# Performance work log

Hardware: AMD Instinct MI355X
Metric: run time of the kernel (lower is better)

## Reference

```python
import jax, jax.numpy as jnp
import numpy as np

N = 20000   # nodes
E = 240000  # edges (avg degree 12)
D = 128     # hidden_dim
H = 4       # heads
C = D // H  # head dim = 32
L = 3       # layers


def _ln(x, g, b):
    m = x.mean(-1, keepdims=True)
    v = ((x - m) ** 2).mean(-1, keepdims=True)
    return (x - m) / jnp.sqrt(v + 1e-5) * g + b


def setup_inputs() -> dict:
    key = jax.random.key(0)
    ks = iter(jax.random.split(key, 64))
    def w(shape, s=0.02):
        return jax.random.normal(next(ks), shape, jnp.float32) * s
    z = lambda shape: jnp.zeros(shape, jnp.float32)
    o = lambda shape: jnp.ones(shape, jnp.float32)
    inp = {
        'xyz': jax.random.normal(next(ks), (N, 3), jnp.float32) * 10.0,
        'attr': jax.random.uniform(next(ks), (N, 1), jnp.float32),
        'edge_index': jax.random.randint(next(ks), (2, E), 0, N, jnp.int32),
        # input encoder
        'enc_W': w((4, D)), 'enc_b': z((D,)), 'enc_g': o((D,)), 'enc_bb': z((D,)),
        # relative position MLP
        'pos_W1': w((3, D)), 'pos_b1': z((D,)), 'pos_g': o((D,)), 'pos_bb': z((D,)),
        'pos_W2': w((D, D)), 'pos_b2': z((D,)),
        # TransformerConv per-layer params (stacked over L)
        'Wq': w((L, D, D)), 'bq': z((L, D)),
        'Wk': w((L, D, D)), 'bk': z((L, D)),
        'Wv': w((L, D, D)), 'bv': z((L, D)),
        'We': w((L, D, D)),                 # lin_edge (no bias in PyG)
        'Wskip': w((L, D, D)), 'bskip': z((L, D)),
        'Wbeta': w((L, 3 * D, 1)),          # lin_beta (no bias)
        'ln1_g': o((L, D)), 'ln1_b': z((L, D)),
        'ln2_g': o((L, D)), 'ln2_b': z((L, D)),
        'fW1': w((L, D, 2 * D)), 'fb1': z((L, 2 * D)),
        'fW2': w((L, 2 * D, D)), 'fb2': z((L, D)),
        # heads
        'cls_W1': w((D, D // 2)), 'cls_b1': z((D // 2,)),
        'cls_W2': w((D // 2, 4)), 'cls_b2': z((4,)),
        'box_W1': w((D, D // 2)), 'box_b1': z((D // 2,)),
        'box_W2': w((D // 2, 7)), 'box_b2': z((7,)),
    }
    return inp


def reference(xyz, attr, edge_index, enc_W, enc_b, enc_g, enc_bb,
              pos_W1, pos_b1, pos_g, pos_bb, pos_W2, pos_b2,
              Wq, bq, Wk, bk, Wv, bv, We, Wskip, bskip, Wbeta,
              ln1_g, ln1_b, ln2_g, ln2_b, fW1, fb1, fW2, fb2,
              cls_W1, cls_b1, cls_W2, cls_b2, box_W1, box_b1, box_W2, box_b2):
    n = xyz.shape[0]
    src, dst = edge_index[0], edge_index[1]  # x_j = x[src], x_i = x[dst]; aggregate at dst
    inv_sqrt_c = 1.0 / float(np.sqrt(C))

    # input encoder: Linear -> LayerNorm -> ReLU
    x = jnp.concatenate([xyz, attr], axis=-1)
    x = jax.nn.relu(_ln(x @ enc_W + enc_b, enc_g, enc_bb))

    # relative position encoding per edge: i, j = edge_index; rel = xyz[j] - xyz[i]
    rel = xyz[dst] - xyz[src]
    e = jax.nn.relu(_ln(rel @ pos_W1 + pos_b1, pos_g, pos_bb)) @ pos_W2 + pos_b2  # [E, D]

    for l in range(L):
        # TransformerConv (beta=True, concat=True, edge_dim=D), eval mode (no dropout)
        q = (x @ Wq[l] + bq[l]).reshape(n, H, C)
        k = (x @ Wk[l] + bk[l]).reshape(n, H, C)
        v = (x @ Wv[l] + bv[l]).reshape(n, H, C)
        ee = (e @ We[l]).reshape(-1, H, C)          # [E, H, C]
        kj = k[src] + ee                             # edge-conditioned keys
        alpha = (q[dst] * kj).sum(-1) * inv_sqrt_c   # [E, H]
        amax = jax.ops.segment_max(alpha, dst, num_segments=n)
        ex = jnp.exp(alpha - amax[dst])
        den = jax.ops.segment_sum(ex, dst, num_segments=n)
        a = ex / den[dst]                            # scatter softmax over in-edges of dst
        msg = (v[src] + ee) * a[:, :, None]
        out = jax.ops.segment_sum(msg, dst, num_segments=n).reshape(n, D)
        # beta-gated skip
        r = x @ Wskip[l] + bskip[l]
        beta = jax.nn.sigmoid(jnp.concatenate([out, r, out - r], axis=-1) @ Wbeta[l])  # [N,1]
        out = beta * r + (1.0 - beta) * out
        # residual + LN + FFN + residual + LN
        x = _ln(out + x, ln1_g[l], ln1_b[l])
        h = jax.nn.gelu(x @ fW1[l] + fb1[l], approximate=False) @ fW2[l] + fb2[l]
        x = _ln(h + x, ln2_g[l], ln2_b[l])

    cls_logits = jax.nn.relu(x @ cls_W1 + cls_b1) @ cls_W2 + cls_b2  # [N, 4]
    box_pred = jax.nn.relu(x @ box_W1 + box_b1) @ box_W2 + box_b2    # [N, 7]
    return (cls_logits, box_pred)
```

## Files before the change

### kernel.cpp

```cpp
#include <hip/hip_runtime.h>
#include <hip/hip_bf16.h>
#include <math.h>

#define DD 128

typedef __attribute__((ext_vector_type(8))) short short8;
typedef __attribute__((ext_vector_type(4))) float f32x4;


__device__ __forceinline__ unsigned short f2b(float f) {
    unsigned u = __float_as_uint(f);
    return (unsigned short)((u + 0x7FFFu + ((u >> 16) & 1u)) >> 16);
}
__device__ __forceinline__ float b2f(unsigned short b) {
    return __uint_as_float(((unsigned)b) << 16);
}
__device__ __forceinline__ unsigned packbf(float a, float b) {
    return (unsigned)f2b(a) | ((unsigned)f2b(b) << 16);
}

__device__ __forceinline__ void redsum2_half(float& a, float& b) {
    #pragma unroll
    for (int off = 32; off > 0; off >>= 1) {
        a += __shfl_down(a, off);
        b += __shfl_down(b, off);
    }
    __shared__ float sa[4], sb4[4];
    int w = threadIdx.x >> 6;
    if ((threadIdx.x & 63) == 0) { sa[w] = a; sb4[w] = b; }
    __syncthreads();
    int h = threadIdx.x >> 7;
    a = sa[2 * h] + sa[2 * h + 1];
    b = sb4[2 * h] + sb4[2 * h + 1];
    __syncthreads();
}

__global__ __launch_bounds__(256) void setup1_kernel(
        const float* __restrict__ xyz, const float* __restrict__ attr,
        const float* __restrict__ encW, const float* __restrict__ encb,
        const float* __restrict__ encg, const float* __restrict__ encbb,
        float* __restrict__ x, unsigned short* __restrict__ xbuf,
        const float* __restrict__ posW1, const float* __restrict__ posb1,
        const float* __restrict__ posg, float* __restrict__ pw,
        const int* __restrict__ ei, int* __restrict__ deg,
        int N, int E, int encBlocks) {
    const int b = blockIdx.x, t = threadIdx.x;
    if (b < encBlocks) {
        const int h = t >> 7, d = t & 127;
        const int node = b * 2 + h;
        const bool ok = node < N;
        __shared__ float sin4[2][4];
        if (ok && d < 3) sin4[h][d] = xyz[node * 3 + d];
        if (ok && d == 3) sin4[h][3] = attr[node];
        __syncthreads();
        float y = encb[d];
        if (ok) {
            #pragma unroll
            for (int kk = 0; kk < 4; ++kk) y += sin4[h][kk] * encW[kk * DD + d];
        }
        float s = y, s2 = y * y;
        redsum2_half(s, s2);
        if (ok) {
            float mean = s * (1.0f / DD);
            float var = s2 * (1.0f / DD) - mean * mean;
            float xn = fmaxf((y - mean) * rsqrtf(var + 1e-5f) * encg[d] + encbb[d], 0.f);
            x[(size_t)node * DD + d] = xn;
            xbuf[(size_t)node * DD + d] = f2b(xn);
        }
    } else if (b == encBlocks) {
        const int d = t & 127;
        float w0 = posW1[d], w1 = posW1[DD + d], w2 = posW1[2 * DD + d], bb = posb1[d];
        float s0 = w0, s1 = w1;
        redsum2_half(s0, s1);
        float s2 = w2, s3 = bb;
        redsum2_half(s2, s3);
        float c0 = w0 - s0 * (1.f / DD), c1 = w1 - s1 * (1.f / DD);
        float c2 = w2 - s2 * (1.f / DD), bc = bb - s3 * (1.f / DD);
        float gd = posg[d];
        pw[d] = c0 * gd; pw[DD + d] = c1 * gd; pw[2 * DD + d] = c2 * gd; pw[3 * DD + d] = bc * gd;
        float p0 = c0 * c0, p1 = c0 * c1; redsum2_half(p0, p1);
        float p2 = c0 * c2, p3 = c1 * c1; redsum2_half(p2, p3);
        float p4 = c1 * c2, p5 = c2 * c2; redsum2_half(p4, p5);
        float p6 = c0 * bc, p7 = c1 * bc; redsum2_half(p6, p7);
        float p8 = c2 * bc, p9 = bc * bc; redsum2_half(p8, p9);
        if ((t & 127) == 0) {
            pw[512] = p0 * (1.f / DD); pw[513] = p1 * (1.f / DD); pw[514] = p2 * (1.f / DD);
            pw[515] = p3 * (1.f / DD); pw[516] = p4 * (1.f / DD); pw[517] = p5 * (1.f / DD);
            pw[518] = p6 * (1.f / DD); pw[519] = p7 * (1.f / DD); pw[520] = p8 * (1.f / DD);
            pw[521] = p9 * (1.f / DD);
        }
    } else {
        int e = (b - encBlocks - 1) * 256 + t;
        if (e < E) atomicAdd(&deg[ei[E + e]], 1);
    }
}

__global__ void scan_kernel(const int* __restrict__ deg, int* __restrict__ ptr, int n) {
    __shared__ int partial[1024];
    int t = threadIdx.x;
    int CH = (n + 1023) >> 10;
    int beg = t * CH;
    int end = beg + CH; if (end > n) end = n;
    int s = 0;
    for (int i = beg; i < end; ++i) s += deg[i];
    partial[t] = s;
    __syncthreads();
    for (int off = 1; off < 1024; off <<= 1) {
        int add = (t >= off) ? partial[t - off] : 0;
        __syncthreads();
        partial[t] += add;
        __syncthreads();
    }
    int base = (t == 0) ? 0 : partial[t - 1];
    for (int i = beg; i < end; ++i) {
        ptr[i] = base;
        base += deg[i];
    }
    if (end == n && beg < n) ptr[n] = base;
}

__global__ __launch_bounds__(256) void setup2_kernel(
        const int* __restrict__ ei, const float* __restrict__ xyz,
        const float* __restrict__ pw, const int* __restrict__ ptr,
        int* __restrict__ cur, int* __restrict__ cs_src, float4* __restrict__ rel4, int E,
        const float* __restrict__ W2, const float* __restrict__ b2,
        const float* __restrict__ We, unsigned* __restrict__ W2Wep, float* __restrict__ b2We,
        const float* __restrict__ Wq, const float* __restrict__ Wk,
        const float* __restrict__ Wv, const float* __restrict__ Ws,
        const float* __restrict__ fW1, const float* __restrict__ fW2,
        unsigned* __restrict__ Wpall,
        const float* __restrict__ cW1, const float* __restrict__ bW1,
        unsigned* __restrict__ Whp,
        const float* __restrict__ cb1, const float* __restrict__ bb1,
        float* __restrict__ b1cat, int SC) {
    const int b = blockIdx.x, t = threadIdx.x;
    if (b < SC) {
        int e = b * 256 + t;
        if (e >= E) return;
        int srcn = ei[e], dstn = ei[E + e];
        int p = atomicAdd(&cur[dstn], 1);
        int slot = ptr[dstn] + p;
        cs_src[slot] = srcn;
        float r0 = xyz[dstn * 3]     - xyz[srcn * 3];
        float r1 = xyz[dstn * 3 + 1] - xyz[srcn * 3 + 1];
        float r2 = xyz[dstn * 3 + 2] - xyz[srcn * 3 + 2];
        float var = pw[512] * r0 * r0 + pw[515] * r1 * r1 + pw[517] * r2 * r2
                  + 2.f * (pw[513] * r0 * r1 + pw[514] * r0 * r2 + pw[516] * r1 * r2)
                  + 2.f * (pw[518] * r0 + pw[519] * r1 + pw[520] * r2) + pw[521];
        rel4[slot] = make_float4(r0, r1, r2, rsqrtf(var + 1e-5f));
        return;
    }
    if (b < SC + 99) {
        int z = b - SC;
        int y = z / 33, bp = z % 33;
        int sub = t >> 7, d = t & 127;
        int bid = bp * 2 + sub;
        const float* We_l = We + (size_t)y * DD * DD;
        __shared__ float s0[2][DD], s1[2][DD];
        if (bid < 64)       { s0[sub][d] = W2[(2 * bid) * DD + d]; s1[sub][d] = W2[(2 * bid + 1) * DD + d]; }
        else if (bid == 64) { s0[sub][d] = b2[d]; s1[sub][d] = 0.f; }
        __syncthreads();
        if (bid <= 64) {
            float a0 = 0.f, a1 = 0.f;
            #pragma unroll 8
            for (int kk = 0; kk < DD; ++kk) {
                float w = We_l[kk * DD + d];
                a0 += s0[sub][kk] * w;
                a1 += s1[sub][kk] * w;
            }
            if (bid < 64) W2Wep[y * 8192 + (((d << 6) + bid) ^ ((d & 7) << 2))] = packbf(a0, a1);
            else          b2We[y * DD + d] = a0;
        }
        return;
    }
    if (b < SC + 99 + 768) {
        int z = b - SC - 99;
        int blob = z >> 5, bp = z & 31;
        int kp = bp * 2 + (t >> 7), d = t & 127;
        float w0, w1;
        if (blob < 12) {
            int l = blob >> 2, wt = blob & 3;
            const float* W = (wt == 0 ? Wq : wt == 1 ? Wk : wt == 2 ? Wv : Ws) + (size_t)l * DD * DD;
            w0 = W[(size_t)(2 * kp) * DD + d];
            w1 = W[(size_t)(2 * kp + 1) * DD + d];
        } else if (blob < 18) {
            int i = blob - 12, l = i >> 1, hf = i & 1;
            const float* W = fW1 + (size_t)l * DD * 256;
            w0 = W[(size_t)(2 * kp) * 256 + hf * 128 + d];
            w1 = W[(size_t)(2 * kp + 1) * 256 + hf * 128 + d];
        } else {
            int i = blob - 18, l = i >> 1, c = i & 1;
            const float* W = fW2 + (size_t)l * 256 * DD;
            w0 = W[(size_t)(c * 128 + 2 * kp) * DD + d];
            w1 = W[(size_t)(c * 128 + 2 * kp + 1) * DD + d];
        }
        Wpall[blob * 8192 + (((d << 6) + kp) ^ ((d & 7) << 2))] = packbf(w0, w1);
        return;
    }
    if (b < SC + 99 + 768 + 32) {
        int bp = b - (SC + 99 + 768);
        int kp = bp * 2 + (t >> 7), d = t & 127;
        int k0 = 2 * kp, k1 = 2 * kp + 1;
        float w0 = (d < 64) ? cW1[k0 * 64 + d] : bW1[k0 * 64 + (d - 64)];
        float w1 = (d < 64) ? cW1[k1 * 64 + d] : bW1[k1 * 64 + (d - 64)];
        Whp[((d << 6) + kp) ^ ((d & 7) << 2)] = packbf(w0, w1);
        return;
    }
    if (t < 128) b1cat[t] = (t < 64) ? cb1[t] : bb1[t - 64];
}

struct B4 { const float* b[4]; };

__global__ __launch_bounds__(256) void proj_kernel(
        const unsigned short* __restrict__ xb, const unsigned* __restrict__ Wp4, B4 bias,
        unsigned short* __restrict__ qkv, float* __restrict__ rbuf, int rowsN, int rtN,
        const float4* __restrict__ rel4, const float* __restrict__ pw,
        const float* __restrict__ bbp, const unsigned* __restrict__ Wpee,
        const float* __restrict__ biasee, unsigned short* __restrict__ eeout,
        int rowsE, int rtE) {
    __shared__ unsigned Bt[8192];
    __shared__ float sc[640];
    const int t = threadIdx.x;
    const int lane = t & 63, wid = t >> 6;
    const int kqo = (lane >> 4) * 8;

    if ((int)blockIdx.x < rtE) {
        const int rowBase = (int)blockIdx.x << 6;
        #pragma unroll
        for (int i = 0; i < 8; ++i)
            *(uint4*)&Bt[(i * 256 + t) * 4] = *(const uint4*)&Wpee[(i * 256 + t) * 4];
        for (int i = t; i < 640; i += 256)
            sc[i] = (i < 512) ? pw[i] : bbp[i - 512];
        int arow = rowBase + wid * 16 + (lane & 15);
        if (arow > rowsE - 1) arow = rowsE - 1;
        float4 rv = rel4[arow];
        __syncthreads();
        short8 a[4];
        #pragma unroll
        for (int kc = 0; kc < 4; ++kc) {
            union { short8 s; unsigned short u[8]; } cv;
            #pragma unroll
            for (int j = 0; j < 8; ++j) {
                int d = kc * 32 + kqo + j;
                float y = fmaf(rv.x, sc[d], fmaf(rv.y, sc[128 + d], fmaf(rv.z, sc[256 + d], sc[384 + d])));
                cv.u[j] = f2b(fmaxf(fmaf(y, rv.w, sc[512 + d]), 0.f));
            }
            a[kc] = cv.s;
        }
        f32x4 acc[8];
        #pragma unroll
        for (int i = 0; i < 8; ++i) acc[i] = (f32x4){0.f, 0.f, 0.f, 0.f};
        #pragma unroll
        for (int ng = 0; ng < 8; ++ng) {
            int col = ng * 16 + (lane & 15);
            #pragma unroll
            for (int kc = 0; kc < 4; ++kc) {
                int kidx = kc * 16 + (lane >> 4) * 4;
                const short8 b = *(const short8*)((const char*)Bt +
                        ((((col << 6) + kidx) ^ ((col & 7) << 2)) << 2));
                acc[ng] = __builtin_amdgcn_mfma_f32_16x16x32_bf16(a[kc], b, acc[ng], 0, 0, 0);
            }
        }
        __syncthreads();
        unsigned short* sb16 = (unsigned short*)Bt;
        #pragma unroll
        for (int ng = 0; ng < 8; ++ng) {
            int col = ng * 16 + (lane & 15);
            float bv = biasee[col];
            int cp = col >> 1, cb = col & 1;
            #pragma unroll
            for (int r = 0; r < 4; ++r) {
                int row = wid * 16 + (lane >> 4) * 4 + r;
                sb16[((row << 6) + (cp ^ ((row & 7) << 2))) * 2 + cb] = f2b(acc[ng][r] + bv);
            }
        }
        __syncthreads();
        unsigned* outw = (unsigned*)eeout;
        #pragma unroll
        for (int i = 0; i < 4; ++i) {
            int j = i * 1024 + t * 4;
            int row = j >> 6, cp = j & 63;
            uint4 v = *(const uint4*)&Bt[(row << 6) + (cp ^ ((row & 7) << 2))];
            int grow = rowBase + row;
            if (grow < rowsE) *(uint4*)&outw[(size_t)grow * 64 + cp] = v;
        }
        return;
    }

    int bidx = (int)blockIdx.x - rtE;
    const int y = bidx / rtN;
    const int rowBase = (bidx % rtN) << 6;
    const unsigned* Wp = Wp4 + y * 8192;
    #pragma unroll
    for (int i = 0; i < 8; ++i)
        *(uint4*)&Bt[(i * 256 + t) * 4] = *(const uint4*)&Wp[(i * 256 + t) * 4];
    int arow = rowBase + wid * 16 + (lane & 15);
    if (arow > rowsN - 1) arow = rowsN - 1;
    short8 a[4];
    #pragma unroll
    for (int kc = 0; kc < 4; ++kc)
        a[kc] = *(const short8*)(xb + (size_t)arow * DD + kc * 32 + kqo);
    __syncthreads();
    f32x4 acc[8];
    #pragma unroll
    for (int i = 0; i < 8; ++i) acc[i] = (f32x4){0.f, 0.f, 0.f, 0.f};
    #pragma unroll
    for (int ng = 0; ng < 8; ++ng) {
        int col = ng * 16 + (lane & 15);
        #pragma unroll
        for (int kc = 0; kc < 4; ++kc) {
            int kidx = kc * 16 + (lane >> 4) * 4;
            const short8 b = *(const short8*)((const char*)Bt +
                    ((((col << 6) + kidx) ^ ((col & 7) << 2)) << 2));
            acc[ng] = __builtin_amdgcn_mfma_f32_16x16x32_bf16(a[kc], b, acc[ng], 0, 0, 0);
        }
    }
    const float* bs = bias.b[y];
    if (y == 3) {
        #pragma unroll
        for (int ng = 0; ng < 8; ++ng) {
            int col = ng * 16 + (lane & 15);
            float bv = bs[col];
            #pragma unroll
            for (int r = 0; r < 4; ++r) {
                int grow = rowBase + wid * 16 + (lane >> 4) * 4 + r;
                if (grow < rowsN) rbuf[(size_t)grow * DD + col] = acc[ng][r] + bv;
            }
        }
        return;
    }
    __syncthreads();
    unsigned short* sb16 = (unsigned short*)Bt;
    #pragma unroll
    for (int ng = 0; ng < 8; ++ng) {
        int col = ng * 16 + (lane & 15);
        float bv = bs[col];
        int cp = col >> 1, cb = col & 1;
        #pragma unroll
        for (int r = 0; r < 4; ++r) {
            int row = wid * 16 + (lane >> 4) * 4 + r;
            sb16[((row << 6) + (cp ^ ((row & 7) << 2))) * 2 + cb] = f2b(acc[ng][r] + bv);
        }
    }
    __syncthreads();
    unsigned* outw = (unsigned*)qkv;
    #pragma unroll
    for (int i = 0; i < 4; ++i) {
        int j = i * 1024 + t * 4;
        int row = j >> 6, cp = j & 63;
        uint4 v = *(const uint4*)&Bt[(row << 6) + (cp ^ ((row & 7) << 2))];
        int grow = rowBase + row;
        if (grow < rowsN) *(uint4*)&outw[(size_t)grow * 192 + (y << 6) + cp] = v;
    }
}

__global__ __launch_bounds__(256) void aggc_kernel(
        const unsigned* __restrict__ qkv, const unsigned* __restrict__ ee,
        const int* __restrict__ ptr, const int* __restrict__ cs_src,
        const float* __restrict__ r, const float* __restrict__ Wb,
        const float* __restrict__ g1, const float* __restrict__ b1,
        float* __restrict__ x, unsigned* __restrict__ xbw, int N) {
    const int wave = threadIdx.x >> 6;
    const int lane = threadIdx.x & 63;
    const int node = blockIdx.x;
    __shared__ float sS[4];
    __shared__ float sA0[4][64];
    __shared__ float sA1[4][64];

    unsigned qp = qkv[(size_t)node * 192 + lane];
    float q0 = b2f((unsigned short)qp), q1 = b2f((unsigned short)(qp >> 16));
    int beg = ptr[node], end = ptr[node + 1];
    float s = 0.f, a0 = 0.f, a1 = 0.f;
    int idx = beg + wave;
    unsigned epN = 0, kpN = 0, vpN = 0;
    if (idx < end) {
        int j = cs_src[idx];
        epN = __builtin_nontemporal_load(&ee[(size_t)idx * 64 + lane]);
        kpN = qkv[(size_t)j * 192 + 64 + lane];
        vpN = qkv[(size_t)j * 192 + 128 + lane];
    }
    for (; idx < end; idx += 4) {
        unsigned ep = epN, kp = kpN, vp = vpN;
        int nidx = idx + 4;
        if (nidx < end) {
            int jn = cs_src[nidx];
            epN = __builtin_nontemporal_load(&ee[(size_t)nidx * 64 + lane]);
            kpN = qkv[(size_t)jn * 192 + 64 + lane];
            vpN = qkv[(size_t)jn * 192 + 128 + lane];
        }
        float e0 = b2f((unsigned short)ep), e1 = b2f((unsigned short)(ep >> 16));
        float kj0 = b2f((unsigned short)kp) + e0;
        float kj1 = b2f((unsigned short)(kp >> 16)) + e1;
        float p = q0 * kj0 + q1 * kj1;
        p += __shfl_xor(p, 1); p += __shfl_xor(p, 2);
        p += __shfl_xor(p, 4); p += __shfl_xor(p, 8);
        float w = __expf(p * 0.17677669529663687f);
        s += w;
        a0 += (b2f((unsigned short)vp) + e0) * w;
        a1 += (b2f((unsigned short)(vp >> 16)) + e1) * w;
    }
    sS[wave] = s;
    sA0[wave][lane] = a0;
    sA1[wave][lane] = a1;
    __syncthreads();
    if (wave != 0) return;
    s  = sS[0] + sS[1] + sS[2] + sS[3];
    a0 = sA0[0][lane] + sA0[1][lane] + sA0[2][lane] + sA0[3][lane];
    a1 = sA1[0][lane] + sA1[1][lane] + sA1[2][lane] + sA1[3][lane];

    float inv_s = (s > 0.f) ? 1.f / s : 0.f;
    float od0 = a0 * inv_s, od1 = a1 * inv_s;
    float2 rd = *(const float2*)&r[(size_t)node * DD + lane * 2];
    float2 wb0 = *(const float2*)&Wb[lane * 2];
    float2 wb1 = *(const float2*)&Wb[DD + lane * 2];
    float2 wb2 = *(const float2*)&Wb[2 * DD + lane * 2];
    float part = od0 * wb0.x + rd.x * wb1.x + (od0 - rd.x) * wb2.x
               + od1 * wb0.y + rd.y * wb1.y + (od1 - rd.y) * wb2.y;
    #pragma unroll
    for (int m = 1; m < 64; m <<= 1) part += __shfl_xor(part, m);
    float beta = 1.f / (1.f + __expf(-part));
    float2 xo = *(const float2*)&x[(size_t)node * DD + lane * 2];
    float t0 = beta * rd.x + (1.f - beta) * od0 + xo.x;
    float t1 = beta * rd.y + (1.f - beta) * od1 + xo.y;
    float ss = t0 + t1, ss2 = t0 * t0 + t1 * t1;
    #pragma unroll
    for (int m = 1; m < 64; m <<= 1) { ss += __shfl_xor(ss, m); ss2 += __shfl_xor(ss2, m); }
    float mean = ss * (1.f / DD);
    float var = ss2 * (1.f / DD) - mean * mean;
    float inv = rsqrtf(var + 1e-5f);
    float2 gg = *(const float2*)&g1[lane * 2];
    float2 bbv = *(const float2*)&b1[lane * 2];
    float2 res;
    res.x = (t0 - mean) * inv * gg.x + bbv.x;
    res.y = (t1 - mean) * inv * gg.y + bbv.y;
    *(float2*)&x[(size_t)node * DD + lane * 2] = res;
    xbw[(size_t)node * 64 + lane] = packbf(res.x, res.y);
}

__global__ __launch_bounds__(256) void ffn_fused(
        const unsigned short* __restrict__ xbin, const unsigned* __restrict__ Wp1,
        const float* __restrict__ b1f, const unsigned* __restrict__ Wp2,
        const float* __restrict__ b2f, const float* __restrict__ g,
        const float* __restrict__ bbn, float* __restrict__ x,
        unsigned short* __restrict__ xb, int rows) {
    __shared__ unsigned Bt[8192];
    __shared__ unsigned h1t[8192];
    const int t = threadIdx.x;
    const int rowBase = blockIdx.x << 6;
    const int lane = t & 63, wid = t >> 6;
    const int kqo = (lane >> 4) * 8;
    int arow = rowBase + wid * 16 + (lane & 15);
    if (arow > rows - 1) arow = rows - 1;

    short8 a[4];
    #pragma unroll
    for (int kc = 0; kc < 4; ++kc)
        a[kc] = *(const short8*)(xbin + (size_t)arow * DD + kc * 32 + kqo);

    unsigned short* h16 = (unsigned short*)h1t;
    for (int half = 0; half < 2; ++half) {
        if (half) __syncthreads();
        const unsigned* Wp = Wp1 + half * 8192;
        #pragma unroll
        for (int i = 0; i < 8; ++i)
            *(uint4*)&Bt[(i * 256 + t) * 4] = *(const uint4*)&Wp[(i * 256 + t) * 4];
        __syncthreads();
        f32x4 acc[8];
        #pragma unroll
        for (int i = 0; i < 8; ++i) acc[i] = (f32x4){0.f, 0.f, 0.f, 0.f};
        #pragma unroll
        for (int ng = 0; ng < 8; ++ng) {
            int col = ng * 16 + (lane & 15);
            #pragma unroll
            for (int kc = 0; kc < 4; ++kc) {
                int kidx = kc * 16 + (lane >> 4) * 4;
                const short8 b = *(const short8*)((const char*)Bt +
                        ((((col << 6) + kidx) ^ ((col & 7) << 2)) << 2));
                acc[ng] = __builtin_amdgcn_mfma_f32_16x16x32_bf16(a[kc], b, acc[ng], 0, 0, 0);
            }
        }
        #pragma unroll
        for (int ng = 0; ng < 8; ++ng) {
            int col = half * 128 + ng * 16 + (lane & 15);
            float bv = b1f[col];
            int cp = col >> 1, cb = col & 1;
            #pragma unroll
            for (int r = 0; r < 4; ++r) {
                int row = wid * 16 + (lane >> 4) * 4 + r;
                float val = acc[ng][r] + bv;
                val = 0.5f * val * (1.f + erff(val * 0.70710678118654752f));
                h16[((row << 7) + (cp ^ ((row & 7) << 2))) * 2 + cb] = f2b(val);
            }
        }
    }
    f32x4 accF[8];
    #pragma unroll
    for (int i = 0; i < 8; ++i) accF[i] = (f32x4){0.f, 0.f, 0.f, 0.f};
    const int lrow = wid * 16 + (lane & 15);
    for (int c = 0; c < 2; ++c) {
        __syncthreads();
        const unsigned* Wp = Wp2 + c * 8192;
        #pragma unroll
        for (int i = 0; i < 8; ++i)
            *(uint4*)&Bt[(i * 256 + t) * 4] = *(const uint4*)&Wp[(i * 256 + t) * 4];
        __syncthreads();
        short8 ah[4];
        #pragma unroll
        for (int kc = 0; kc < 4; ++kc) {
            int cp4 = c * 64 + kc * 16 + (lane >> 4) * 4;
            ah[kc] = *(const short8*)&h1t[(lrow << 7) + (cp4 ^ ((lrow & 7) << 2))];
        }
        #pragma unroll
        for (int ng = 0; ng < 8; ++ng) {
            int col = ng * 16 + (lane & 15);
            #pragma unroll
            for (int kc = 0; kc < 4; ++kc) {
                int kidx = kc * 16 + (lane >> 4) * 4;
                const short8 b = *(const short8*)((const char*)Bt +
                        ((((col << 6) + kidx) ^ ((col & 7) << 2)) << 2));
                accF[ng] = __builtin_amdgcn_mfma_f32_16x16x32_bf16(ah[kc], b, accF[ng], 0, 0, 0);
            }
        }
    }
    float tt[8][4];
    float rs[4] = {0.f, 0.f, 0.f, 0.f}, rs2[4] = {0.f, 0.f, 0.f, 0.f};
    #pragma unroll
    for (int ng = 0; ng < 8; ++ng) {
        int col = ng * 16 + (lane & 15);
        float bv = b2f[col];
        #pragma unroll
        for (int r = 0; r < 4; ++r) {
            int grow = rowBase + wid * 16 + (lane >> 4) * 4 + r;
            float xo = (grow < rows) ? x[(size_t)grow * DD + col] : 0.f;
            float v = accF[ng][r] + bv + xo;
            tt[ng][r] = v;
            rs[r] += v;
            rs2[r] += v * v;
        }
    }
    #pragma unroll
    for (int r = 0; r < 4; ++r) {
        #pragma unroll
        for (int m = 1; m < 16; m <<= 1) {
            rs[r] += __shfl_xor(rs[r], m);
            rs2[r] += __shfl_xor(rs2[r], m);
        }
    }
    __syncthreads();
    unsigned short* sb16 = (unsigned short*)Bt;
    #pragma unroll
    for (int ng = 0; ng < 8; ++ng) {
        int col = ng * 16 + (lane & 15);
        float gg = g[col], bbb = bbn[col];
        int cp = col >> 1, cb = col & 1;
        #pragma unroll
        for (int r = 0; r < 4; ++r) {
            int grow = rowBase + wid * 16 + (lane >> 4) * 4 + r;
            float mean = rs[r] * (1.f / DD);
            float var = rs2[r] * (1.f / DD) - mean * mean;
            float val = (tt[ng][r] - mean) * rsqrtf(var + 1e-5f) * gg + bbb;
            if (grow < rows) x[(size_t)grow * DD + col] = val;
            int row = wid * 16 + (lane >> 4) * 4 + r;
            sb16[((row << 6) + (cp ^ ((row & 7) << 2))) * 2 + cb] = f2b(val);
        }
    }
    __syncthreads();
    unsigned* outw = (unsigned*)xb;
    #pragma unroll
    for (int i = 0; i < 4; ++i) {
        int j = i * 1024 + t * 4;
        int row = j >> 6, cp = j & 63;
        uint4 v = *(const uint4*)&Bt[(row << 6) + (cp ^ ((row & 7) << 2))];
        int grow = rowBase + row;
        if (grow < rows) *(uint4*)&outw[(size_t)grow * 64 + cp] = v;
    }
}

__global__ __launch_bounds__(256) void heads_fused(
        const unsigned short* __restrict__ xb, const unsigned* __restrict__ Whp,
        const float* __restrict__ b1cat, const float* __restrict__ cW2,
        const float* __restrict__ cb2, const float* __restrict__ bW2,
        const float* __restrict__ bb2, float* __restrict__ outc,
        float* __restrict__ outb, int rows) {
    __shared__ unsigned Bt[8192];
    __shared__ unsigned ht[4096];
    const int t = threadIdx.x;
    const int rowBase = blockIdx.x << 6;
    const int lane = t & 63, wid = t >> 6;
    const int kqo = (lane >> 4) * 8;
    #pragma unroll
    for (int i = 0; i < 8; ++i)
        *(uint4*)&Bt[(i * 256 + t) * 4] = *(const uint4*)&Whp[(i * 256 + t) * 4];
    int arow = rowBase + wid * 16 + (lane & 15);
    if (arow > rows - 1) arow = rows - 1;
    short8 a[4];
    #pragma unroll
    for (int kc = 0; kc < 4; ++kc)
        a[kc] = *(const short8*)(xb + (size_t)arow * DD + kc * 32 + kqo);
    __syncthreads();
    f32x4 acc[8];
    #pragma unroll
    for (int i = 0; i < 8; ++i) acc[i] = (f32x4){0.f, 0.f, 0.f, 0.f};
    #pragma unroll
    for (int ng = 0; ng < 8; ++ng) {
        int col = ng * 16 + (lane & 15);
        #pragma unroll
        for (int kc = 0; kc < 4; ++kc) {
            int kidx = kc * 16 + (lane >> 4) * 4;
            const short8 b = *(const short8*)((const char*)Bt +
                    ((((col << 6) + kidx) ^ ((col & 7) << 2)) << 2));
            acc[ng] = __builtin_amdgcn_mfma_f32_16x16x32_bf16(a[kc], b, acc[ng], 0, 0, 0);
        }
    }
    unsigned short* h16 = (unsigned short*)ht;
    #pragma unroll
    for (int ng = 0; ng < 8; ++ng) {
        int col = ng * 16 + (lane & 15);
        float bv = b1cat[col];
        int cp = col >> 1, cb = col & 1;
        #pragma unroll
        for (int r = 0; r < 4; ++r) {
            int row = wid * 16 + (lane >> 4) * 4 + r;
            h16[((row << 6) + (cp ^ ((row & 7) << 2))) * 2 + cb] = f2b(fmaxf(acc[ng][r] + bv, 0.f));
        }
    }
    __syncthreads();
    for (int i = t; i < 704; i += 256) {
        int n = i / 11, j = i % 11;
        int grow = rowBase + n;
        if (grow >= rows) continue;
        int sw = (n & 7) << 2;
        if (j < 4) {
            float accv = cb2[j];
            #pragma unroll 8
            for (int kp = 0; kp < 32; ++kp) {
                unsigned w = ht[(n << 6) + (kp ^ sw)];
                accv += b2f((unsigned short)w) * cW2[(2 * kp) * 4 + j];
                accv += b2f((unsigned short)(w >> 16)) * cW2[(2 * kp + 1) * 4 + j];
            }
            outc[(size_t)grow * 4 + j] = accv;
        } else {
            int jj = j - 4;
            float accv = bb2[jj];
            #pragma unroll 8
            for (int kp = 0; kp < 32; ++kp) {
                unsigned w = ht[(n << 6) + ((32 + kp) ^ sw)];
                accv += b2f((unsigned short)w) * bW2[(2 * kp) * 7 + jj];
                accv += b2f((unsigned short)(w >> 16)) * bW2[(2 * kp + 1) * 7 + jj];
            }
            outb[(size_t)grow * 7 + jj] = accv;
        }
    }
}

extern "C" void kernel_launch(void* const* d_in, const int* in_sizes, int n_in,
                              void* d_out, int out_size, void* d_ws, size_t ws_size,
                              hipStream_t stream) {
    const float* xyz   = (const float*)d_in[0];
    const float* attr  = (const float*)d_in[1];
    const int*   ei    = (const int*)d_in[2];
    const float* encW  = (const float*)d_in[3];
    const float* encb  = (const float*)d_in[4];
    const float* encg  = (const float*)d_in[5];
    const float* encbb = (const float*)d_in[6];
    const float* posW1 = (const float*)d_in[7];
    const float* posb1 = (const float*)d_in[8];
    const float* posg  = (const float*)d_in[9];
    const float* posbb = (const float*)d_in[10];
    const float* posW2 = (const float*)d_in[11];
    const float* posb2 = (const float*)d_in[12];
    const float* Wq    = (const float*)d_in[13];
    const float* bq    = (const float*)d_in[14];
    const float* Wk    = (const float*)d_in[15];
    const float* bk    = (const float*)d_in[16];
    const float* Wv    = (const float*)d_in[17];
    const float* bv    = (const float*)d_in[18];
    const float* We    = (const float*)d_in[19];
    const float* Wskip = (const float*)d_in[20];
    const float* bskip = (const float*)d_in[21];
    const float* Wbeta = (const float*)d_in[22];
    const float* ln1g  = (const float*)d_in[23];
    const float* ln1b  = (const float*)d_in[24];
    const float* ln2g  = (const float*)d_in[25];
    const float* ln2b  = (const float*)d_in[26];
    const float* fW1   = (const float*)d_in[27];
    const float* fb1   = (const float*)d_in[28];
    const float* fW2   = (const float*)d_in[29];
    const float* fb2   = (const float*)d_in[30];
    const float* cW1   = (const float*)d_in[31];
    const float* cb1   = (const float*)d_in[32];
    const float* cW2   = (const float*)d_in[33];
    const float* cb2   = (const float*)d_in[34];
    const float* bW1   = (const float*)d_in[35];
    const float* bb1   = (const float*)d_in[36];
    const float* bW2   = (const float*)d_in[37];
    const float* bb2   = (const float*)d_in[38];

    const int N = in_sizes[0] / 3;
    const int E = in_sizes[2] / 2;

    size_t off = 0;
    auto alloc = [&](size_t nelem) {
        char* p = (char*)d_ws + off;
        off += nelem * sizeof(float);
        return (float*)p;
    };
    float* x     = alloc((size_t)N * DD);
    unsigned short* qkv = (unsigned short*)alloc((size_t)N * 192);
    float* r     = alloc((size_t)N * DD);
    unsigned short* xb = (unsigned short*)alloc((size_t)N * 64);
    float4* rel4 = (float4*)alloc((size_t)E * 4);
    unsigned short* eeb = (unsigned short*)alloc((size_t)E * 64);
    unsigned* W2Wep = (unsigned*)alloc(3 * 8192);
    float* b2We  = alloc(3 * DD);
    unsigned* Wpall = (unsigned*)alloc(24 * 8192);
    unsigned* Whp   = (unsigned*)alloc(8192);
    float* pw    = alloc(544);
    float* b1cat = alloc(DD);
    int* deg     = (int*)alloc(N);
    int* cur     = (int*)alloc(N);
    int* ptr     = (int*)alloc(N + 1);
    int* cs_src  = (int*)alloc(E);

    const int rtN = (N + 63) / 64;
    const int rtE = (E + 63) / 64;
    const int encBlocks = (N + 1) / 2;
    const int SC = (E + 255) / 256;

    hipMemsetAsync(deg, 0, 2 * (size_t)N * sizeof(int), stream);
    setup1_kernel<<<encBlocks + 1 + SC, 256, 0, stream>>>(
        xyz, attr, encW, encb, encg, encbb, x, xb,
        posW1, posb1, posg, pw, ei, deg, N, E, encBlocks);
    scan_kernel<<<1, 1024, 0, stream>>>(deg, ptr, N);
    setup2_kernel<<<SC + 99 + 768 + 32 + 1, 256, 0, stream>>>(
        ei, xyz, pw, ptr, cur, cs_src, rel4, E,
        posW2, posb2, We, W2Wep, b2We,
        Wq, Wk, Wv, Wskip, fW1, fW2, Wpall,
        cW1, bW1, Whp, cb1, bb1, b1cat, SC);

    for (int l = 0; l < 3; ++l) {
        const float* Wb_l = Wbeta + (size_t)l * 3 * DD;
        B4 bs;
        bs.b[0] = bq + l * DD; bs.b[1] = bk + l * DD;
        bs.b[2] = bv + l * DD; bs.b[3] = bskip + l * DD;

        proj_kernel<<<rtE + 4 * rtN, 256, 0, stream>>>(
            xb, Wpall + (size_t)l * 4 * 8192, bs, qkv, r, N, rtN,
            rel4, pw, posbb, W2Wep + l * 8192, b2We + l * DD, eeb, E, rtE);

        aggc_kernel<<<N, 256, 0, stream>>>((const unsigned*)qkv, (const unsigned*)eeb,
                                           ptr, cs_src, r, Wb_l,
                                           ln1g + l * DD, ln1b + l * DD,
                                           x, (unsigned*)xb, N);

        ffn_fused<<<rtN, 256, 0, stream>>>(xb, Wpall + (size_t)(12 + 2 * l) * 8192,
                                           fb1 + l * 256, Wpall + (size_t)(18 + 2 * l) * 8192,
                                           fb2 + l * DD, ln2g + l * DD, ln2b + l * DD,
                                           x, xb, N);
    }

    float* outc  = (float*)d_out;
    float* outbx = (float*)d_out + (size_t)N * 4;
    heads_fused<<<rtN, 256, 0, stream>>>(xb, Whp, b1cat, cW2, cb2, bW2, bb2,
                                         outc, outbx, N);
}
```

Measured before the change: 371.7 us.

## Halve FFN row tile and split output columns across wave pairs

The fused FFN kernel now handles 32 rows per block instead of 64. Each pair of waves shares 16 rows and each wave computes half the output columns. LayerNorm row statistics are combined across the two waves through shared memory. This doubles the grid and reduces LDS and register use per block to improve occupancy and load balance. The cost is that each weight tile loaded into LDS is reused over half as many rows, which doubles total weight traffic.

```diff
diff --git a/kernel.cpp b/kernel.cpp
--- a/kernel.cpp
+++ b/kernel.cpp
@@ -444,12 +444,15 @@
         const float* __restrict__ bbn, float* __restrict__ x,
         unsigned short* __restrict__ xb, int rows) {
     __shared__ unsigned Bt[8192];
-    __shared__ unsigned h1t[8192];
+    __shared__ unsigned h1t[4096];
+    __shared__ float sRS[4][16], sRS2[4][16];
     const int t = threadIdx.x;
-    const int rowBase = blockIdx.x << 6;
+    const int rowBase = blockIdx.x << 5;
     const int lane = t & 63, wid = t >> 6;
+    const int wrow = (wid >> 1) * 16;
+    const int wcol = (wid & 1) * 64;
     const int kqo = (lane >> 4) * 8;
-    int arow = rowBase + wid * 16 + (lane & 15);
+    int arow = rowBase + wrow + (lane & 15);
     if (arow > rows - 1) arow = rows - 1;
 
     short8 a[4];
@@ -465,12 +468,12 @@
         for (int i = 0; i < 8; ++i)
             *(uint4*)&Bt[(i * 256 + t) * 4] = *(const uint4*)&Wp[(i * 256 + t) * 4];
         __syncthreads();
-        f32x4 acc[8];
-        #pragma unroll
-        for (int i = 0; i < 8; ++i) acc[i] = (f32x4){0.f, 0.f, 0.f, 0.f};
-        #pragma unroll
-        for (int ng = 0; ng < 8; ++ng) {
-            int col = ng * 16 + (lane & 15);
+        f32x4 acc[4];
+        #pragma unroll
+        for (int i = 0; i < 4; ++i) acc[i] = (f32x4){0.f, 0.f, 0.f, 0.f};
+        #pragma unroll
+        for (int ng = 0; ng < 4; ++ng) {
+            int col = wcol + ng * 16 + (lane & 15);
             #pragma unroll
             for (int kc = 0; kc < 4; ++kc) {
                 int kidx = kc * 16 + (lane >> 4) * 4;
@@ -480,23 +483,23 @@
             }
         }
         #pragma unroll
-        for (int ng = 0; ng < 8; ++ng) {
-            int col = half * 128 + ng * 16 + (lane & 15);
+        for (int ng = 0; ng < 4; ++ng) {
+            int col = half * 128 + wcol + ng * 16 + (lane & 15);
             float bv = b1f[col];
             int cp = col >> 1, cb = col & 1;
             #pragma unroll
             for (int r = 0; r < 4; ++r) {
-                int row = wid * 16 + (lane >> 4) * 4 + r;
+                int row = wrow + (lane >> 4) * 4 + r;
                 float val = acc[ng][r] + bv;
                 val = 0.5f * val * (1.f + erff(val * 0.70710678118654752f));
                 h16[((row << 7) + (cp ^ ((row & 7) << 2))) * 2 + cb] = f2b(val);
             }
         }
     }
-    f32x4 accF[8];
-    #pragma unroll
-    for (int i = 0; i < 8; ++i) accF[i] = (f32x4){0.f, 0.f, 0.f, 0.f};
-    const int lrow = wid * 16 + (lane & 15);
+    f32x4 accF[4];
+    #pragma unroll
+    for (int i = 0; i < 4; ++i) accF[i] = (f32x4){0.f, 0.f, 0.f, 0.f};
+    const int lrow = wrow + (lane & 15);
     for (int c = 0; c < 2; ++c) {
         __syncthreads();
         const unsigned* Wp = Wp2 + c * 8192;
@@ -511,8 +514,8 @@
             ah[kc] = *(const short8*)&h1t[(lrow << 7) + (cp4 ^ ((lrow & 7) << 2))];
         }
         #pragma unroll
-        for (int ng = 0; ng < 8; ++ng) {
-            int col = ng * 16 + (lane & 15);
+        for (int ng = 0; ng < 4; ++ng) {
+            int col = wcol + ng * 16 + (lane & 15);
             #pragma unroll
             for (int kc = 0; kc < 4; ++kc) {
                 int kidx = kc * 16 + (lane >> 4) * 4;
@@ -522,15 +525,15 @@
             }
         }
     }
-    float tt[8][4];
+    float tt[4][4];
     float rs[4] = {0.f, 0.f, 0.f, 0.f}, rs2[4] = {0.f, 0.f, 0.f, 0.f};
     #pragma unroll
-    for (int ng = 0; ng < 8; ++ng) {
-        int col = ng * 16 + (lane & 15);
+    for (int ng = 0; ng < 4; ++ng) {
+        int col = wcol + ng * 16 + (lane & 15);
         float bv = b2f[col];
         #pragma unroll
         for (int r = 0; r < 4; ++r) {
-            int grow = rowBase + wid * 16 + (lane >> 4) * 4 + r;
+            int grow = rowBase + wrow + (lane >> 4) * 4 + r;
             float xo = (grow < rows) ? x[(size_t)grow * DD + col] : 0.f;
             float v = accF[ng][r] + bv + xo;
             tt[ng][r] = v;
@@ -546,33 +549,43 @@
             rs2[r] += __shfl_xor(rs2[r], m);
         }
     }
+    if ((lane & 15) == 0) {
+        #pragma unroll
+        for (int r = 0; r < 4; ++r) {
+            sRS[wid][(lane >> 4) * 4 + r] = rs[r];
+            sRS2[wid][(lane >> 4) * 4 + r] = rs2[r];
+        }
+    }
     __syncthreads();
     unsigned short* sb16 = (unsigned short*)Bt;
     #pragma unroll
-    for (int ng = 0; ng < 8; ++ng) {
-        int col = ng * 16 + (lane & 15);
+    for (int ng = 0; ng < 4; ++ng) {
+        int col = wcol + ng * 16 + (lane & 15);
         float gg = g[col], bbb = bbn[col];
         int cp = col >> 1, cb = col & 1;
         #pragma unroll
         for (int r = 0; r < 4; ++r) {
-            int grow = rowBase + wid * 16 + (lane >> 4) * 4 + r;
-            float mean = rs[r] * (1.f / DD);
-            float var = rs2[r] * (1.f / DD) - mean * mean;
+            int ri = (lane >> 4) * 4 + r;
+            float st = sRS[wid][ri] + sRS[wid ^ 1][ri];
+            float st2 = sRS2[wid][ri] + sRS2[wid ^ 1][ri];
+            int grow = rowBase + wrow + ri;
+            float mean = st * (1.f / DD);
+            float var = st2 * (1.f / DD) - mean * mean;
             float val = (tt[ng][r] - mean) * rsqrtf(var + 1e-5f) * gg + bbb;
             if (grow < rows) x[(size_t)grow * DD + col] = val;
-            int row = wid * 16 + (lane >> 4) * 4 + r;
+            int row = wrow + ri;
             sb16[((row << 6) + (cp ^ ((row & 7) << 2))) * 2 + cb] = f2b(val);
         }
     }
     __syncthreads();
     unsigned* outw = (unsigned*)xb;
     #pragma unroll
-    for (int i = 0; i < 4; ++i) {
-        int j = i * 1024 + t * 4;
-        int row = j >> 6, cp = j & 63;
-        uint4 v = *(const uint4*)&Bt[(row << 6) + (cp ^ ((row & 7) << 2))];
+    for (int i = 0; i < 2; ++i) {
+        int j = i * 256 + t;
+        int row = j >> 4, c4 = j & 15;
+        uint4 v = *(const uint4*)&Bt[(row << 6) + ((c4 << 2) ^ ((row & 7) << 2))];
         int grow = rowBase + row;
-        if (grow < rows) *(uint4*)&outw[(size_t)grow * 64 + cp] = v;
+        if (grow < rows) *(uint4*)&outw[(size_t)grow * 64 + (c4 << 2)] = v;
     }
 }
 
@@ -723,6 +736,7 @@
     int* cs_src  = (int*)alloc(E);
 
     const int rtN = (N + 63) / 64;
+    const int rtN2 = (N + 31) / 32;
     const int rtE = (E + 63) / 64;
     const int encBlocks = (N + 1) / 2;
     const int SC = (E + 255) / 256;
@@ -753,10 +767,10 @@
                                            ln1g + l * DD, ln1b + l * DD,
                                            x, (unsigned*)xb, N);
 
-        ffn_fused<<<rtN, 256, 0, stream>>>(xb, Wpall + (size_t)(12 + 2 * l) * 8192,
-                                           fb1 + l * 256, Wpall + (size_t)(18 + 2 * l) * 8192,
-                                           fb2 + l * DD, ln2g + l * DD, ln2b + l * DD,
-                                           x, xb, N);
+        ffn_fused<<<rtN2, 256, 0, stream>>>(xb, Wpall + (size_t)(12 + 2 * l) * 8192,
+                                            fb1 + l * 256, Wpall + (size_t)(18 + 2 * l) * 8192,
+                                            fb2 + l * DD, ln2g + l * DD, ln2b + l * DD,
+                                            x, xb, N);
     }
 
     float* outc  = (float*)d_out;
```

Measured after the change: 364.3 us. -2.0%, faster.
